# Kernel tuning notes

Hardware: AMD Instinct MI355X
Metric: run time of the kernel (lower is better)

The kernel has to match this reference:

```python
import jax, jax.numpy as jnp
import numpy as np

B, L, D, H = 16, 1024, 768, 12
PHD = D // H  # per-head dim = 64


def setup_inputs() -> dict:
    key = jax.random.key(0)
    ks = jax.random.split(key, 6)
    s = 0.02  # small init scale (xavier-like magnitude)
    return {
        "embeddings": jax.random.normal(ks[0], (B, L, D), jnp.float32),
        "pre_w": jax.random.normal(ks[1], (D, D), jnp.float32) * s,
        "pre_b": jnp.zeros((D,), jnp.float32),
        "psfs": jax.random.normal(ks[2], (H, 2 * L - 1, PHD), jnp.float32) * s,
        "post_w": jax.random.normal(ks[3], (D, D), jnp.float32) * s,
        "post_b": jnp.zeros((D,), jnp.float32),
        "sparse_mat": jax.random.normal(ks[4], (L, L), jnp.float32) * s,
        "ln_g": jnp.ones((D,), jnp.float32),
        "ln_b": jnp.zeros((D,), jnp.float32),
    }


def _spectral_norm(W, n_iters=1, eps=1e-12):
    # torch spectral_norm: power iteration with detached u, v; sigma = u^T W v
    u = jnp.ones((W.shape[0],), W.dtype) / jnp.sqrt(jnp.asarray(W.shape[0], W.dtype))
    for _ in range(n_iters):
        v = W.T @ u
        v = v / (jnp.linalg.norm(v) + eps)
        u = W @ v
        u = u / (jnp.linalg.norm(u) + eps)
    u = jax.lax.stop_gradient(u)
    v = jax.lax.stop_gradient(v)
    sigma = u @ (W @ v)
    return W / sigma


def reference(embeddings, pre_w, pre_b, psfs, post_w, post_b, sparse_mat, ln_g, ln_b):
    # pre-projection
    x = embeddings @ pre_w.T + pre_b                       # (B, L, D)
    # zero-pad along seq to 2L-1 and split heads
    xp = jnp.pad(x, ((0, 0), (0, L - 1), (0, 0)))          # (B, 2L-1, D)
    xp = xp.reshape(B, 2 * L - 1, H, PHD).transpose(0, 2, 1, 3)  # (B, H, 2L-1, d)
    # causal PSF mask: keep first L taps, zero the rest (zeros still enter softmax, as in torch)
    causal = (jnp.arange(2 * L - 1) < L)[None, :, None]
    psf = jnp.where(causal, psfs, 0.0)                     # (H, 2L-1, d)
    psf = jax.nn.softmax(psf, axis=1)
    # 2D circular convolution via FFT over (seq, head_dim)
    conv = jnp.fft.ifftn(jnp.fft.fftn(psf, axes=(1, 2))[None] * jnp.fft.fftn(xp, axes=(2, 3)), axes=(2, 3))
    conv = jnp.real(conv)[:, :, :L, :]                     # (B, H, L, d)
    conv = jax.nn.gelu(conv, approximate=False).transpose(0, 2, 1, 3).reshape(B, L, D)
    conv_emb = conv @ post_w.T + post_b
    # sparse branch: spectrally-normalized, causal-masked dense mixing matrix
    sp = jnp.tril(_spectral_norm(sparse_mat))              # (L, L)
    sparse_emb = jnp.einsum('st,btd->bsd', sp, x)
    # dropout is identity (eval), keep_prob = 1.0; residual + LayerNorm(eps=1e-12)
    y = conv_emb + sparse_emb + embeddings
    mu = jnp.mean(y, axis=-1, keepdims=True)
    var = jnp.mean((y - mu) ** 2, axis=-1, keepdims=True)
    return (y - mu) * jax.lax.rsqrt(var + 1e-12) * ln_g + ln_b
```

## Files before the change

### kernel.cpp

```cpp
#include <hip/hip_runtime.h>
#include <math.h>

#define Bn 16
#define Ln 1024
#define Dn 768
#define Hn 12
#define PHDn 64
#define NK 33
#define NHK (Hn * NK)
#define TWOPI_64 0.09817477042468103f

typedef short s16x8 __attribute__((ext_vector_type(8)));
typedef float f32x4 __attribute__((ext_vector_type(4)));
typedef unsigned short u16x4 __attribute__((ext_vector_type(4)));

__device__ __forceinline__ unsigned short f2bf(float f) {
    unsigned int u = __float_as_uint(f);
    unsigned int r = (u + 0x7FFFu + ((u >> 16) & 1u)) >> 16;
    return (unsigned short)r;
}
__device__ __forceinline__ float bf2f(unsigned short s) {
    unsigned int u = ((unsigned int)s) << 16;
    return __uint_as_float(u);
}
__device__ __forceinline__ float2 cmul(float2 a, float2 b) {
    return make_float2(a.x * b.x - a.y * b.y, a.x * b.y + a.y * b.x);
}

#define SW(j) ((j) ^ (((j) >> 2) & 12) ^ (((j) >> 6) & 3))

static const size_t O_P    = 0;
static const size_t O_PSFH = 786432;
static const size_t O_PART = 1376256;
static const size_t O_QH   = 1597440;
static const size_t O_X    = 1598240;
static const size_t O_XH   = 14181152;
static const size_t O_YH   = 27157280;
static const size_t O_SPE  = 40146080;
static const size_t O_V    = 52728992;
static const size_t O_UR   = 52730016;
static const size_t O_SIG  = 52731040;

__global__ __launch_bounds__(256) void k_psf_softmax(const float* __restrict__ psfs,
                                                     float* __restrict__ p,
                                                     float* __restrict__ q) {
    int he = blockIdx.x;
    int h = he >> 6, e = he & 63;
    int tid = threadIdx.x;
    float ev[4];
    float s = 0.f;
#pragma unroll
    for (int i = 0; i < 4; ++i) {
        int t = tid + 256 * i;
        float v = psfs[((size_t)h * 2047 + t) * 64 + e];
        ev[i] = expf(v);
        s += ev[i];
    }
    __shared__ float red[256];
    red[tid] = s; __syncthreads();
    for (int st = 128; st > 0; st >>= 1) {
        if (tid < st) red[tid] += red[tid + st];
        __syncthreads();
    }
    float denom = red[0] + 1023.0f;
    float inv = 1.0f / denom;
#pragma unroll
    for (int i = 0; i < 4; ++i) {
        int t = tid + 256 * i;
        p[((size_t)h * 1024 + t) * 64 + e] = ev[i] * inv;
    }
    if (tid == 0) q[he] = inv;
}

__global__ __launch_bounds__(256) void k_psf_dft(const float* __restrict__ p,
                                                 float* __restrict__ psfh) {
    int blk = blockIdx.x;
    int h = blk >> 8, tb = blk & 255;
    int t0 = tb * 4;
    int tid = threadIdx.x;
    int w = tid >> 6, lane = tid & 63;
    __shared__ float pv[4][64], cc[64], ssn[64];
    if (tid < 64) {
        float ang = TWOPI_64 * tid;
        cc[tid] = cosf(ang); ssn[tid] = sinf(ang);
    }
    pv[w][lane] = p[((size_t)h * 1024 + t0 + w) * 64 + lane];
    __syncthreads();
    if (lane < NK) {
        float re = 0.f, im = 0.f;
#pragma unroll 8
        for (int e = 0; e < 64; ++e) {
            int j = (lane * e) & 63;
            float v = pv[w][e];
            re += v * cc[j];
            im -= v * ssn[j];
        }
        size_t o = (((size_t)h * NK + lane) * 1024 + t0 + w) * 2;
        psfh[o] = re; psfh[o + 1] = im;
    }
}

__global__ __launch_bounds__(64) void k_q_dft(const float* __restrict__ q,
                                              float* __restrict__ qh) {
    int h = blockIdx.x;
    int tid = threadIdx.x;
    __shared__ float qv[64], cc[64], ssn[64];
    qv[tid] = q[h * 64 + tid];
    float ang = TWOPI_64 * tid;
    cc[tid] = cosf(ang); ssn[tid] = sinf(ang);
    __syncthreads();
    if (tid < NK) {
        float re = 0.f, im = 0.f;
        for (int e = 0; e < 64; ++e) {
            int j = (tid * e) & 63;
            re += qv[e] * cc[j];
            im -= qv[e] * ssn[j];
        }
        qh[(h * NK + tid) * 2] = re;
        qh[(h * NK + tid) * 2 + 1] = im;
    }
}

__device__ __forceinline__ void build_twiddles(float2* tw, int tid) {
#pragma unroll
    for (int it = 0; it < 2; ++it) {
        int j = tid + it * 256;
        float a = (float)j * 3.0679615757712823e-3f;
        float sv, cv;
        __sincosf(a, &sv, &cv);
        tw[j] = make_float2(cv, -sv);
    }
}

__device__ __forceinline__ void fft_pair(const float2* __restrict__ X,
                                         float2* __restrict__ Y,
                                         const float2* __restrict__ tw,
                                         int tid, int m) {
#pragma unroll
    for (int it = 0; it < 2; ++it) {
        int i = tid + it * 256;
        int r = i & (m - 1);
        int am = i - r;
        float2 w1 = tw[am];
        float2 w1b = make_float2(w1.y, -w1.x);
        float2 w2 = cmul(w1, w1);
        float2 x0 = X[SW(i)], x1 = X[SW(i + 512)], x2 = X[SW(i + 1024)], x3 = X[SW(i + 1536)];
        float2 y0 = make_float2(x0.x + x2.x, x0.y + x2.y);
        float2 y1 = cmul(make_float2(x0.x - x2.x, x0.y - x2.y), w1);
        float2 y2 = make_float2(x1.x + x3.x, x1.y + x3.y);
        float2 y3 = cmul(make_float2(x1.x - x3.x, x1.y - x3.y), w1b);
        int o = 4 * am + r;
        Y[SW(o)] = make_float2(y0.x + y2.x, y0.y + y2.y);
        Y[SW(o + m)] = make_float2(y1.x + y3.x, y1.y + y3.y);
        Y[SW(o + 2 * m)] = cmul(make_float2(y0.x - y2.x, y0.y - y2.y), w2);
        Y[SW(o + 3 * m)] = cmul(make_float2(y1.x - y3.x, y1.y - y3.y), w2);
    }
}

__global__ __launch_bounds__(256) void k_tap_fft(const float* __restrict__ psfh,
                                                 const float* __restrict__ qh,
                                                 float* __restrict__ phf) {
    __shared__ float2 A[2048], B[2048], tw[512];
    int hk = blockIdx.x, tid = threadIdx.x;
    build_twiddles(tw, tid);
    float2 qv = make_float2(qh[hk * 2], qh[hk * 2 + 1]);
    const float2* Pg = (const float2*)(psfh + (size_t)hk * 2048);
    __syncthreads();
#pragma unroll
    for (int it = 0; it < 2; ++it) {
        int i = tid + it * 256;
        float2 x0 = Pg[i], x1 = Pg[i + 512];
        float2 x2 = (i == 0) ? make_float2(0.f, 0.f) : qv;
        float2 x3 = qv;
        float2 w1 = tw[i];
        float2 w1b = make_float2(w1.y, -w1.x);
        float2 w2 = cmul(w1, w1);
        float2 y0 = make_float2(x0.x + x2.x, x0.y + x2.y);
        float2 y1 = cmul(make_float2(x0.x - x2.x, x0.y - x2.y), w1);
        float2 y2 = make_float2(x1.x + x3.x, x1.y + x3.y);
        float2 y3 = cmul(make_float2(x1.x - x3.x, x1.y - x3.y), w1b);
        int o = 4 * i;
        A[SW(o)] = make_float2(y0.x + y2.x, y0.y + y2.y);
        A[SW(o + 1)] = make_float2(y1.x + y3.x, y1.y + y3.y);
        A[SW(o + 2)] = cmul(make_float2(y0.x - y2.x, y0.y - y2.y), w2);
        A[SW(o + 3)] = cmul(make_float2(y1.x - y3.x, y1.y - y3.y), w2);
    }
    __syncthreads();
    fft_pair(A, B, tw, tid, 4);   __syncthreads();
    fft_pair(B, A, tw, tid, 16);  __syncthreads();
    fft_pair(A, B, tw, tid, 64);  __syncthreads();
    fft_pair(B, A, tw, tid, 256); __syncthreads();
    float2* out = (float2*)(phf + (size_t)hk * 4096);
#pragma unroll
    for (int it = 0; it < 4; ++it) {
        int t = tid + it * 256;
        float2 lo = A[SW(t)], hi = A[SW(t + 1024)];
        out[t] = make_float2(lo.x + hi.x, lo.y + hi.y);
        out[t + 1024] = make_float2(lo.x - hi.x, lo.y - hi.y);
    }
}

__global__ __launch_bounds__(256) void k_conv_fft(const float* __restrict__ XH,
                                                  const float* __restrict__ PHF,
                                                  float* __restrict__ YH) {
    __shared__ float2 A[2048], B[2048], tw[512];
    int bhk = blockIdx.x, tid = threadIdx.x;
    int hk = bhk % NHK;
    build_twiddles(tw, tid);
    const float2* Xg = (const float2*)(XH + (size_t)bhk * 2048);
    __syncthreads();
#pragma unroll
    for (int it = 0; it < 2; ++it) {
        int i = tid + it * 256;
        float2 x0 = Xg[i];
        float2 x1 = Xg[i + 512];
        float2 w1 = tw[i];
        float2 w1b = make_float2(w1.y, -w1.x);
        float2 w2 = cmul(w1, w1);
        float2 y1 = cmul(x0, w1);
        float2 y3 = cmul(x1, w1b);
        int o = 4 * i;
        A[SW(o)] = make_float2(x0.x + x1.x, x0.y + x1.y);
        A[SW(o + 1)] = make_float2(y1.x + y3.x, y1.y + y3.y);
        A[SW(o + 2)] = cmul(make_float2(x0.x - x1.x, x0.y - x1.y), w2);
        A[SW(o + 3)] = cmul(make_float2(y1.x - y3.x, y1.y - y3.y), w2);
    }
    __syncthreads();
    fft_pair(A, B, tw, tid, 4);   __syncthreads();
    fft_pair(B, A, tw, tid, 16);  __syncthreads();
    fft_pair(A, B, tw, tid, 64);  __syncthreads();
    fft_pair(B, A, tw, tid, 256); __syncthreads();
    const float2* P = (const float2*)(PHF + (size_t)hk * 4096);
    float2 q[8];
#pragma unroll
    for (int it = 0; it < 4; ++it) {
        int t = tid + it * 256;
        float2 lo = A[SW(t)], hi = A[SW(t + 1024)];
        float2 fl = make_float2(lo.x + hi.x, lo.y + hi.y);
        float2 fh = make_float2(lo.x - hi.x, lo.y - hi.y);
        float2 vl = cmul(fl, P[t]);
        float2 vh = cmul(fh, P[t + 1024]);
        q[it] = make_float2(vl.x, -vl.y);
        q[it + 4] = make_float2(vh.x, -vh.y);
    }
#pragma unroll
    for (int it = 0; it < 2; ++it) {
        int i = tid + it * 256;
        float2 x0 = q[it], x1 = q[it + 2], x2 = q[it + 4], x3 = q[it + 6];
        float2 w1 = tw[i];
        float2 w1b = make_float2(w1.y, -w1.x);
        float2 w2 = cmul(w1, w1);
        float2 y0 = make_float2(x0.x + x2.x, x0.y + x2.y);
        float2 y1 = cmul(make_float2(x0.x - x2.x, x0.y - x2.y), w1);
        float2 y2 = make_float2(x1.x + x3.x, x1.y + x3.y);
        float2 y3 = cmul(make_float2(x1.x - x3.x, x1.y - x3.y), w1b);
        int o = 4 * i;
        B[SW(o)] = make_float2(y0.x + y2.x, y0.y + y2.y);
        B[SW(o + 1)] = make_float2(y1.x + y3.x, y1.y + y3.y);
        B[SW(o + 2)] = cmul(make_float2(y0.x - y2.x, y0.y - y2.y), w2);
        B[SW(o + 3)] = cmul(make_float2(y1.x - y3.x, y1.y - y3.y), w2);
    }
    __syncthreads();
    fft_pair(B, A, tw, tid, 4);   __syncthreads();
    fft_pair(A, B, tw, tid, 16);  __syncthreads();
    fft_pair(B, A, tw, tid, 64);  __syncthreads();
    fft_pair(A, B, tw, tid, 256); __syncthreads();
    float2* Yg = (float2*)(YH + (size_t)bhk * 2048);
    const float inv_n = 1.0f / 2048.0f;
#pragma unroll
    for (int it = 0; it < 4; ++it) {
        int s = tid + it * 256;
        float2 lo = B[SW(s)], hi = B[SW(s + 1024)];
        Yg[s] = make_float2((lo.x + hi.x) * inv_n, -(lo.y + hi.y) * inv_n);
    }
}

__global__ __launch_bounds__(64) void k_build_wf1(unsigned short* __restrict__ W) {
    int m = blockIdx.x;
    int d = threadIdx.x;
    float val = 0.f;
    if (m < 66) {
        int k = m >> 1, od = m & 1;
        int j = (k * d) & 63;
        float ang = TWOPI_64 * (float)j;
        val = od ? -sinf(ang) : cosf(ang);
    }
    W[m * 64 + d] = f2bf(val);
}

__global__ __launch_bounds__(64) void k_build_wi1(unsigned short* __restrict__ W) {
    int m = blockIdx.x;
    int c = threadIdx.x;
    float val = 0.f;
    if (m < 64) {
        int d = m;
        int k, od;
        float ck;
        if (c == 0)      { k = 0;  od = 0; ck = 1.f / 64.f; }
        else if (c == 1) { k = 32; od = 0; ck = 1.f / 64.f; }
        else             { k = c >> 1; od = c & 1; ck = 2.f / 64.f; }
        int j = (k * d) & 63;
        float ang = TWOPI_64 * (float)j;
        val = od ? -sinf(ang) * ck : cosf(ang) * ck;
    }
    W[m * 64 + c] = f2bf(val);
}

__device__ __forceinline__ void mfma_core64(const unsigned short* __restrict__ gA0,
                                            const unsigned short* __restrict__ gB0,
                                            int nkt,
                                            unsigned short* __restrict__ As,
                                            unsigned short* __restrict__ Bs,
                                            int tid, int lane, int wr, int wc,
                                            f32x4 acc[4][4]) {
    int r0 = tid >> 1, hs = (tid & 1) << 2;
    int wbase = r0 * 64;
    int swr = r0 & 7;
    int kg = lane >> 4, cl = lane & 15;
    int fra[8], frb[8];
#pragma unroll
    for (int kk = 0; kk < 2; ++kk)
#pragma unroll
        for (int i = 0; i < 4; ++i) {
            int ra = wr * 64 + i * 16 + cl;
            fra[kk * 4 + i] = ra * 64 + (((kk * 4 + kg) ^ (ra & 7)) << 3);
            int rb = wc * 64 + i * 16 + cl;
            frb[kk * 4 + i] = rb * 64 + (((kk * 4 + kg) ^ (rb & 7)) << 3);
        }
    s16x8 a[4], b[4];
#pragma unroll
    for (int l = 0; l < 4; ++l) {
        a[l] = *(const s16x8*)(gA0 + l * 8);
        b[l] = *(const s16x8*)(gB0 + l * 8);
    }
    for (int kt = 0; kt < nkt; ++kt) {
        __syncthreads();
#pragma unroll
        for (int l = 0; l < 4; ++l) {
            *(s16x8*)&As[wbase + (((hs + l) ^ swr) << 3)] = a[l];
            *(s16x8*)&Bs[wbase + (((hs + l) ^ swr) << 3)] = b[l];
        }
        __syncthreads();
        if (kt + 1 < nkt) {
            size_t ko = (size_t)(kt + 1) * 64;
#pragma unroll
            for (int l = 0; l < 4; ++l) {
                a[l] = *(const s16x8*)(gA0 + ko + l * 8);
                b[l] = *(const s16x8*)(gB0 + ko + l * 8);
            }
        }
#pragma unroll
        for (int kk = 0; kk < 2; ++kk) {
            s16x8 af[4], bfr[4];
#pragma unroll
            for (int i = 0; i < 4; ++i) af[i] = *(const s16x8*)&As[fra[kk * 4 + i]];
#pragma unroll
            for (int i = 0; i < 4; ++i) bfr[i] = *(const s16x8*)&Bs[frb[kk * 4 + i]];
#pragma unroll
            for (int mi = 0; mi < 4; ++mi)
#pragma unroll
                for (int ni = 0; ni < 4; ++ni)
                    acc[mi][ni] = __builtin_amdgcn_mfma_f32_16x16x32_bf16(af[mi], bfr[ni], acc[mi][ni], 0, 0, 0);
        }
    }
}

__global__ __launch_bounds__(256) void k_mfma_abt_bf(const unsigned short* __restrict__ A,
                                                     const unsigned short* __restrict__ W,
                                                     const float* __restrict__ bias,
                                                     unsigned short* __restrict__ C,
                                                     int M, int N, int K) {
    int n0 = blockIdx.x * 128, m0 = blockIdx.y * 128;
    int tid = threadIdx.x;
    int lane = tid & 63, wave = tid >> 6;
    int wr = wave >> 1, wc = wave & 1;
    __shared__ __align__(16) unsigned short As[8192], Bs[8192];
    f32x4 acc[4][4] = {};
    int r0 = tid >> 1, hs = (tid & 1) << 2;
    const unsigned short* gA0 = A + (size_t)(m0 + r0) * K + hs * 8;
    const unsigned short* gB0 = W + (size_t)(n0 + r0) * K + hs * 8;
    mfma_core64(gA0, gB0, K >> 6, As, Bs, tid, lane, wr, wc, acc);
    int kg = lane >> 4, cl = lane & 15;
#pragma unroll
    for (int ni = 0; ni < 4; ++ni) {
        int gn = n0 + wc * 64 + ni * 16 + cl;
        float bv = bias ? bias[gn] : 0.f;
#pragma unroll
        for (int mi = 0; mi < 4; ++mi) {
            int gm = m0 + wr * 64 + mi * 16 + kg * 4;
            f32x4 v = acc[mi][ni];
#pragma unroll
            for (int ri = 0; ri < 4; ++ri)
                C[(size_t)(gm + ri) * N + gn] = f2bf(v[ri] + bv);
        }
    }
}

__global__ __launch_bounds__(256) void k_mfma_dft_h(const unsigned short* __restrict__ Wf1,
                                                    const unsigned short* __restrict__ Xb,
                                                    float* __restrict__ XH) {
    int n0 = blockIdx.x * 128;
    int h = blockIdx.y;
    int tid = threadIdx.x;
    int lane = tid & 63, wave = tid >> 6;
    int wr = wave >> 1, wc = wave & 1;
    __shared__ __align__(16) unsigned short As[8192], Bs[8192];
    f32x4 acc[4][4] = {};
    int r0 = tid >> 1, hs = (tid & 1) << 2;
    const unsigned short* gA0 = Wf1 + r0 * 64 + hs * 8;
    const unsigned short* gB0 = Xb + (size_t)(n0 + r0) * Dn + h * 64 + hs * 8;
    mfma_core64(gA0, gB0, 1, As, Bs, tid, lane, wr, wc, acc);
    int kg = lane >> 4, cl = lane & 15;
#pragma unroll
    for (int ni = 0; ni < 4; ++ni) {
        int gn = n0 + wc * 64 + ni * 16 + cl;
        int b = gn >> 10, u = gn & 1023;
#pragma unroll
        for (int mi = 0; mi < 4; ++mi) {
            int gmb = wr * 64 + mi * 16 + kg * 4;
            f32x4 v = acc[mi][ni];
#pragma unroll
            for (int rp = 0; rp < 2; ++rp) {
                int m = gmb + rp * 2;
                if (m < 66) {
                    size_t plane = (size_t)(b * Hn + h) * NK + (m >> 1);
                    *(float2*)&XH[(plane * 1024 + u) * 2] = make_float2(v[rp * 2], v[rp * 2 + 1]);
                }
            }
        }
    }
}

__global__ __launch_bounds__(256) void k_transpose_yh(const float* __restrict__ YH,
                                                      unsigned short* __restrict__ YT) {
    int ut = blockIdx.x & 7;
    int h = (blockIdx.x >> 3) % 12;
    int b = blockIdx.x / 96;
    int u0 = ut * 128;
    __shared__ unsigned short T[128 * 66];
    int tid = threadIdx.x;
    int planeBase = (b * Hn + h) * NK;
    const float2* Yg = (const float2*)YH;
#pragma unroll
    for (int i = 0; i < 17; ++i) {
        int idx = tid + i * 256;
        if (idx < 4224) {
            int k = idx >> 7, uo = idx & 127;
            float2 v = Yg[(size_t)(planeBase + k) * 1024 + u0 + uo];
            T[uo * 66 + 2 * k] = f2bf(v.x);
            T[uo * 66 + 2 * k + 1] = f2bf(v.y);
        }
    }
    __syncthreads();
    unsigned int* out = (unsigned int*)YT;
#pragma unroll
    for (int i = 0; i < 16; ++i) {
        int idx = tid + i * 256;
        int uo = idx >> 5, w = idx & 31;
        unsigned int lo, hi;
        if (w == 0) {
            lo = T[uo * 66 + 0];
            hi = T[uo * 66 + 64];
        } else {
            lo = T[uo * 66 + 2 * w];
            hi = T[uo * 66 + 2 * w + 1];
        }
        size_t r = (size_t)b * 1024 + u0 + uo;
        out[r * 384 + h * 32 + w] = lo | (hi << 16);
    }
}

__global__ __launch_bounds__(256) void k_mfma_idft_h(const unsigned short* __restrict__ YT,
                                                     const unsigned short* __restrict__ Wi1,
                                                     unsigned short* __restrict__ G) {
    int m0 = blockIdx.x * 128;
    int h = blockIdx.y;
    int tid = threadIdx.x;
    int lane = tid & 63, wave = tid >> 6;
    int wr = wave >> 1, wc = wave & 1;
    __shared__ __align__(16) unsigned short As[8192], Bs[8192];
    f32x4 acc[4][4] = {};
    int r0 = tid >> 1, hs = (tid & 1) << 2;
    const unsigned short* gA0 = YT + (size_t)(m0 + r0) * Dn + h * 64 + hs * 8;
    const unsigned short* gB0 = Wi1 + r0 * 64 + hs * 8;
    mfma_core64(gA0, gB0, 1, As, Bs, tid, lane, wr, wc, acc);
    int kg = lane >> 4, cl = lane & 15;
#pragma unroll
    for (int ni = 0; ni < 4; ++ni) {
        int gn = wc * 64 + ni * 16 + cl;
        if (gn < 64) {
#pragma unroll
            for (int mi = 0; mi < 4; ++mi) {
                int gm = m0 + wr * 64 + mi * 16 + kg * 4;
                f32x4 v = acc[mi][ni];
#pragma unroll
                for (int ri = 0; ri < 4; ++ri) {
                    float c = v[ri];
                    float g = c * 0.5f * (1.0f + erff(c * 0.70710678118f));
                    G[(size_t)(gm + ri) * Dn + h * 64 + gn] = f2bf(g);
                }
            }
        }
    }
}

__global__ __launch_bounds__(256) void k_mfma_sparse(const unsigned short* __restrict__ SP,
                                                     const unsigned short* __restrict__ XT,
                                                     const float* __restrict__ sigbuf,
                                                     unsigned short* __restrict__ C) {
    int bx = blockIdx.x;
    int mt = bx & 7, nt = (bx >> 3) % 6, b = bx / 48;
    int m0 = mt * 128, n0 = nt * 128;
    const unsigned short* Xb = XT + (size_t)b * Dn * Ln;
    unsigned short* Cb = C + (size_t)b * Ln * Dn;
    int tid = threadIdx.x;
    int lane = tid & 63, wave = tid >> 6;
    int wr = wave >> 1, wc = wave & 1;
    __shared__ __align__(16) unsigned short As[8192], Bs[8192];
    f32x4 acc[4][4] = {};
    int r0 = tid >> 1, hs = (tid & 1) << 2;
    const unsigned short* gA0 = SP + (size_t)(m0 + r0) * Ln + hs * 8;
    const unsigned short* gB0 = Xb + (size_t)(n0 + r0) * Ln + hs * 8;
    mfma_core64(gA0, gB0, 2 * mt + 2, As, Bs, tid, lane, wr, wc, acc);
    float invs = sigbuf[0];
    int kg = lane >> 4, cl = lane & 15;
#pragma unroll
    for (int ni = 0; ni < 4; ++ni) {
        int gn = n0 + wc * 64 + ni * 16 + cl;
#pragma unroll
        for (int mi = 0; mi < 4; ++mi) {
            int gm = m0 + wr * 64 + mi * 16 + kg * 4;
            f32x4 v = acc[mi][ni];
#pragma unroll
            for (int ri = 0; ri < 4; ++ri)
                Cb[(size_t)(gm + ri) * Dn + gn] = f2bf(v[ri] * invs);
        }
    }
}

__global__ __launch_bounds__(256) void k_cvt_bf16(const float* __restrict__ in,
                                                  unsigned short* __restrict__ out, int n4) {
    int i = blockIdx.x * 256 + threadIdx.x;
    if (i < n4) {
        float4 v = ((const float4*)in)[i];
        u16x4 o;
        o[0] = f2bf(v.x); o[1] = f2bf(v.y); o[2] = f2bf(v.z); o[3] = f2bf(v.w);
        *(u16x4*)&out[(size_t)i * 4] = o;
    }
}

__global__ __launch_bounds__(256) void k_cvt_sp(const float* __restrict__ SP,
                                                unsigned short* __restrict__ O) {
    int s = blockIdx.x;
    int t0 = threadIdx.x * 4;
    float4 v = *(const float4*)&SP[(size_t)s * 1024 + t0];
    u16x4 o;
    o[0] = (t0 + 0 <= s) ? f2bf(v.x) : 0;
    o[1] = (t0 + 1 <= s) ? f2bf(v.y) : 0;
    o[2] = (t0 + 2 <= s) ? f2bf(v.z) : 0;
    o[3] = (t0 + 3 <= s) ? f2bf(v.w) : 0;
    *(u16x4*)&O[(size_t)s * 1024 + t0] = o;
}

__global__ __launch_bounds__(256) void k_transpose_x(const unsigned short* __restrict__ X,
                                                     unsigned short* __restrict__ XT) {
    int d0 = blockIdx.x * 64, t0 = blockIdx.y * 64, b = blockIdx.z;
    const unsigned short* Xb = X + (size_t)b * Ln * Dn;
    unsigned short* Tb = XT + (size_t)b * Dn * Ln;
    __shared__ unsigned short tile[64 * 65];
    int tx = threadIdx.x & 63, ty = threadIdx.x >> 6;
#pragma unroll
    for (int i = 0; i < 16; ++i) {
        int t = ty + i * 4;
        tile[t * 65 + tx] = Xb[(size_t)(t0 + t) * Dn + d0 + tx];
    }
    __syncthreads();
#pragma unroll
    for (int i = 0; i < 16; ++i) {
        int d = ty + i * 4;
        Tb[(size_t)(d0 + d) * Ln + t0 + tx] = tile[tx * 65 + d];
    }
}

__global__ __launch_bounds__(256) void k_sn_colsum(const float* __restrict__ Wm,
                                                   float* __restrict__ partial) {
    int b = blockIdx.x;
    int tid = threadIdx.x;
    int c0 = tid * 4;
    float4 s = make_float4(0.f, 0.f, 0.f, 0.f);
#pragma unroll
    for (int i = 0; i < 16; ++i) {
        float4 v = *(const float4*)&Wm[(size_t)(b * 16 + i) * 1024 + c0];
        s.x += v.x; s.y += v.y; s.z += v.z; s.w += v.w;
    }
    *(float4*)&partial[(size_t)b * 1024 + c0] = s;
}

__global__ __launch_bounds__(1024) void k_sn_v2(const float* __restrict__ partial,
                                                float* __restrict__ v) {
    int j = threadIdx.x;
    float s = 0.f;
#pragma unroll 8
    for (int i = 0; i < 64; ++i) s += partial[(size_t)i * 1024 + j];
    s *= 0.03125f;
    __shared__ float red[1024];
    red[j] = s * s; __syncthreads();
    for (int st = 512; st > 0; st >>= 1) {
        if (j < st) red[j] += red[j + st];
        __syncthreads();
    }
    float nrm = sqrtf(red[0]);
    v[j] = s / (nrm + 1e-12f);
}

__global__ __launch_bounds__(64) void k_sn_u(const float* __restrict__ Wm,
                                             const float* __restrict__ v,
                                             float* __restrict__ ur) {
    int i = blockIdx.x;
    int lane = threadIdx.x;
    float s = 0.f;
    for (int j = lane; j < 1024; j += 64) s += Wm[(size_t)i * 1024 + j] * v[j];
#pragma unroll
    for (int off = 32; off > 0; off >>= 1) s += __shfl_down(s, off);
    if (lane == 0) ur[i] = s;
}

__global__ __launch_bounds__(1024) void k_sn_sigma(const float* __restrict__ ur,
                                                   float* __restrict__ sig) {
    int i = threadIdx.x;
    __shared__ float red[1024];
    float u = ur[i];
    red[i] = u * u; __syncthreads();
    for (int st = 512; st > 0; st >>= 1) {
        if (i < st) red[i] += red[i + st];
        __syncthreads();
    }
    if (i == 0) {
        float ss = red[0];
        float sigma = ss / (sqrtf(ss) + 1e-12f);
        sig[0] = 1.0f / sigma;
    }
}

__global__ __launch_bounds__(256) void k_final_ln(const unsigned short* __restrict__ CE,
                                                  const unsigned short* __restrict__ SE,
                                                  const float* __restrict__ EMB,
                                                  const float* __restrict__ g,
                                                  const float* __restrict__ be,
                                                  float* __restrict__ out) {
    int r = blockIdx.x;
    int tid = threadIdx.x;
    float y[3];
    float s = 0.f;
#pragma unroll
    for (int i = 0; i < 3; ++i) {
        int o = tid + i * 256;
        size_t idx = (size_t)r * 768 + o;
        y[i] = bf2f(CE[idx]) + bf2f(SE[idx]) + EMB[idx];
        s += y[i];
    }
    __shared__ float red[256];
    red[tid] = s; __syncthreads();
    for (int st = 128; st > 0; st >>= 1) {
        if (tid < st) red[tid] += red[tid + st];
        __syncthreads();
    }
    float mu = red[0] * (1.f / 768.f);
    __syncthreads();
    float vs = 0.f;
#pragma unroll
    for (int i = 0; i < 3; ++i) { float d = y[i] - mu; vs += d * d; }
    red[tid] = vs; __syncthreads();
    for (int st = 128; st > 0; st >>= 1) {
        if (tid < st) red[tid] += red[tid + st];
        __syncthreads();
    }
    float var = red[0] * (1.f / 768.f);
    float rstd = rsqrtf(var + 1e-12f);
#pragma unroll
    for (int i = 0; i < 3; ++i) {
        int o = tid + i * 256;
        size_t idx = (size_t)r * 768 + o;
        out[idx] = (y[i] - mu) * rstd * g[o] + be[o];
    }
}

extern "C" void kernel_launch(void* const* d_in, const int* in_sizes, int n_in,
                              void* d_out, int out_size, void* d_ws, size_t ws_size,
                              hipStream_t stream) {
    const float* emb     = (const float*)d_in[0];
    const float* pre_w   = (const float*)d_in[1];
    const float* pre_b   = (const float*)d_in[2];
    const float* psfs    = (const float*)d_in[3];
    const float* post_w  = (const float*)d_in[4];
    const float* post_b  = (const float*)d_in[5];
    const float* spmat   = (const float*)d_in[6];
    const float* ln_g    = (const float*)d_in[7];
    const float* ln_b    = (const float*)d_in[8];
    float* out = (float*)d_out;
    float* ws = (float*)d_ws;

    float* p      = ws + O_P;
    float* psfh   = ws + O_PSFH;
    float* part   = ws + O_PART;
    float* qh     = ws + O_QH;
    float* q      = ws + O_SIG + 8;
    float* XH     = ws + O_XH;
    float* YH     = ws + O_YH;
    float* phf    = ws + O_SPE;
    float* v      = ws + O_V;
    float* urw    = ws + O_UR;
    float* sig    = ws + O_SIG;

    unsigned short* x_bf      = (unsigned short*)(ws + O_X);
    unsigned short* Wf1       = (unsigned short*)(ws + O_X + 6291456);
    unsigned short* Wi1       = (unsigned short*)(ws + O_X + 6295552);
    unsigned short* YT        = (unsigned short*)(ws + O_XH);
    unsigned short* xT_bf     = (unsigned short*)(ws + O_XH);
    unsigned short* emb_bf    = (unsigned short*)(ws + O_YH);
    unsigned short* CE_bf     = (unsigned short*)(ws + O_YH);
    unsigned short* spe_bf    = (unsigned short*)(ws + O_SPE);
    unsigned short* G_bf      = (unsigned short*)(ws + O_SPE + 3145728);
    unsigned short* SP_bf     = (unsigned short*)(ws + O_P);
    unsigned short* pre_w_bf  = (unsigned short*)(ws + O_PSFH);
    unsigned short* post_w_bf = (unsigned short*)(ws + O_PSFH + 294912);

    k_psf_softmax<<<Hn * 64, 256, 0, stream>>>(psfs, p, q);
    k_psf_dft<<<Hn * 256, 256, 0, stream>>>(p, psfh);
    k_q_dft<<<Hn, 64, 0, stream>>>(q, qh);
    k_tap_fft<<<NHK, 256, 0, stream>>>(psfh, qh, phf);

    k_sn_colsum<<<64, 256, 0, stream>>>(spmat, part);
    k_sn_v2<<<1, 1024, 0, stream>>>(part, v);
    k_sn_u<<<1024, 64, 0, stream>>>(spmat, v, urw);
    k_sn_sigma<<<1, 1024, 0, stream>>>(urw, sig);

    k_cvt_sp<<<1024, 256, 0, stream>>>(spmat, SP_bf);
    k_cvt_bf16<<<576, 256, 0, stream>>>(pre_w, pre_w_bf, 147456);
    k_cvt_bf16<<<576, 256, 0, stream>>>(post_w, post_w_bf, 147456);
    k_cvt_bf16<<<12288, 256, 0, stream>>>(emb, emb_bf, 3145728);
    k_build_wf1<<<128, 64, 0, stream>>>(Wf1);
    k_build_wi1<<<128, 64, 0, stream>>>(Wi1);

    k_mfma_abt_bf<<<dim3(6, 128), 256, 0, stream>>>(emb_bf, pre_w_bf, pre_b, x_bf, Bn * Ln, Dn, Dn);

    k_mfma_dft_h<<<dim3(128, Hn), 256, 0, stream>>>(Wf1, x_bf, XH);

    k_conv_fft<<<Bn * NHK, 256, 0, stream>>>(XH, phf, YH);

    k_transpose_yh<<<Bn * Hn * 8, 256, 0, stream>>>(YH, YT);

    k_mfma_idft_h<<<dim3(128, Hn), 256, 0, stream>>>(YT, Wi1, G_bf);

    k_transpose_x<<<dim3(12, 16, Bn), 256, 0, stream>>>(x_bf, xT_bf);

    k_mfma_abt_bf<<<dim3(6, 128), 256, 0, stream>>>(G_bf, post_w_bf, post_b, CE_bf, Bn * Ln, Dn, Dn);

    k_mfma_sparse<<<768, 256, 0, stream>>>(SP_bf, xT_bf, sig, spe_bf);

    k_final_ln<<<Bn * Ln, 256, 0, stream>>>(CE_bf, spe_bf, emb, ln_g, ln_b, out);
}
```

Baseline: 319.5 us.

## Store FFT spectra as packed bf16 and fuse fp32→bf16 conversion into GEMM loads

Intermediate frequency-domain buffers XH and YH are now stored as packed bf16 complex pairs instead of float2, halving the memory traffic of the DFT, convolution FFT and transpose kernels. The separate fp32-to-bf16 conversion kernels for embeddings and the pre/post weights are removed; the GEMM loaders read fp32 directly and convert in registers. This trades extra spectral rounding error and some redundant fp32 global reads for fewer kernel launches and less intermediate traffic.

```diff
diff --git a/kernel.cpp b/kernel.cpp
--- a/kernel.cpp
+++ b/kernel.cpp
@@ -25,6 +25,12 @@
 }
 __device__ __forceinline__ float2 cmul(float2 a, float2 b) {
     return make_float2(a.x * b.x - a.y * b.y, a.x * b.y + a.y * b.x);
+}
+__device__ __forceinline__ unsigned int packbf(float re, float im) {
+    return (unsigned int)f2bf(re) | ((unsigned int)f2bf(im) << 16);
+}
+__device__ __forceinline__ float2 unpackbf(unsigned int v) {
+    return make_float2(bf2f((unsigned short)(v & 0xffff)), bf2f((unsigned short)(v >> 16)));
 }
 
 #define SW(j) ((j) ^ (((j) >> 2) & 12) ^ (((j) >> 6) & 3))
@@ -200,20 +206,20 @@
     }
 }
 
-__global__ __launch_bounds__(256) void k_conv_fft(const float* __restrict__ XH,
+__global__ __launch_bounds__(256) void k_conv_fft(const unsigned int* __restrict__ XHb,
                                                   const float* __restrict__ PHF,
-                                                  float* __restrict__ YH) {
+                                                  unsigned int* __restrict__ YHb) {
     __shared__ float2 A[2048], B[2048], tw[512];
     int bhk = blockIdx.x, tid = threadIdx.x;
     int hk = bhk % NHK;
     build_twiddles(tw, tid);
-    const float2* Xg = (const float2*)(XH + (size_t)bhk * 2048);
+    const unsigned int* Xg = XHb + (size_t)bhk * 1024;
     __syncthreads();
 #pragma unroll
     for (int it = 0; it < 2; ++it) {
         int i = tid + it * 256;
-        float2 x0 = Xg[i];
-        float2 x1 = Xg[i + 512];
+        float2 x0 = unpackbf(Xg[i]);
+        float2 x1 = unpackbf(Xg[i + 512]);
         float2 w1 = tw[i];
         float2 w1b = make_float2(w1.y, -w1.x);
         float2 w2 = cmul(w1, w1);
@@ -265,13 +271,13 @@
     fft_pair(A, B, tw, tid, 16);  __syncthreads();
     fft_pair(B, A, tw, tid, 64);  __syncthreads();
     fft_pair(A, B, tw, tid, 256); __syncthreads();
-    float2* Yg = (float2*)(YH + (size_t)bhk * 2048);
+    unsigned int* Yg = YHb + (size_t)bhk * 1024;
     const float inv_n = 1.0f / 2048.0f;
 #pragma unroll
     for (int it = 0; it < 4; ++it) {
         int s = tid + it * 256;
         float2 lo = B[SW(s)], hi = B[SW(s + 1024)];
-        Yg[s] = make_float2((lo.x + hi.x) * inv_n, -(lo.y + hi.y) * inv_n);
+        Yg[s] = packbf((lo.x + hi.x) * inv_n, -(lo.y + hi.y) * inv_n);
     }
 }
 
@@ -306,8 +312,19 @@
     W[m * 64 + c] = f2bf(val);
 }
 
-__device__ __forceinline__ void mfma_core64(const unsigned short* __restrict__ gA0,
-                                            const unsigned short* __restrict__ gB0,
+__device__ __forceinline__ s16x8 load8(const unsigned short* p) { return *(const s16x8*)p; }
+__device__ __forceinline__ s16x8 load8(const float* p) {
+    float4 u = *(const float4*)p;
+    float4 v = *(const float4*)(p + 4);
+    s16x8 r;
+    r[0] = (short)f2bf(u.x); r[1] = (short)f2bf(u.y); r[2] = (short)f2bf(u.z); r[3] = (short)f2bf(u.w);
+    r[4] = (short)f2bf(v.x); r[5] = (short)f2bf(v.y); r[6] = (short)f2bf(v.z); r[7] = (short)f2bf(v.w);
+    return r;
+}
+
+template <typename TA, typename TB>
+__device__ __forceinline__ void mfma_core64(const TA* __restrict__ gA0,
+                                            const TB* __restrict__ gB0,
                                             int nkt,
                                             unsigned short* __restrict__ As,
                                             unsigned short* __restrict__ Bs,
@@ -330,8 +347,8 @@
     s16x8 a[4], b[4];
 #pragma unroll
     for (int l = 0; l < 4; ++l) {
-        a[l] = *(const s16x8*)(gA0 + l * 8);
-        b[l] = *(const s16x8*)(gB0 + l * 8);
+        a[l] = load8(gA0 + l * 8);
+        b[l] = load8(gB0 + l * 8);
     }
     for (int kt = 0; kt < nkt; ++kt) {
         __syncthreads();
@@ -345,8 +362,8 @@
             size_t ko = (size_t)(kt + 1) * 64;
 #pragma unroll
             for (int l = 0; l < 4; ++l) {
-                a[l] = *(const s16x8*)(gA0 + ko + l * 8);
-                b[l] = *(const s16x8*)(gB0 + ko + l * 8);
+                a[l] = load8(gA0 + ko + l * 8);
+                b[l] = load8(gB0 + ko + l * 8);
             }
         }
 #pragma unroll
@@ -365,11 +382,42 @@
     }
 }
 
-__global__ __launch_bounds__(256) void k_mfma_abt_bf(const unsigned short* __restrict__ A,
-                                                     const unsigned short* __restrict__ W,
-                                                     const float* __restrict__ bias,
-                                                     unsigned short* __restrict__ C,
-                                                     int M, int N, int K) {
+__global__ __launch_bounds__(256) void k_mfma_pre(const float* __restrict__ A,
+                                                  const float* __restrict__ W,
+                                                  const float* __restrict__ bias,
+                                                  unsigned short* __restrict__ C) {
+    const int K = Dn, N = Dn;
+    int n0 = blockIdx.x * 128, m0 = blockIdx.y * 128;
+    int tid = threadIdx.x;
+    int lane = tid & 63, wave = tid >> 6;
+    int wr = wave >> 1, wc = wave & 1;
+    __shared__ __align__(16) unsigned short As[8192], Bs[8192];
+    f32x4 acc[4][4] = {};
+    int r0 = tid >> 1, hs = (tid & 1) << 2;
+    const float* gA0 = A + (size_t)(m0 + r0) * K + hs * 8;
+    const float* gB0 = W + (size_t)(n0 + r0) * K + hs * 8;
+    mfma_core64(gA0, gB0, K >> 6, As, Bs, tid, lane, wr, wc, acc);
+    int kg = lane >> 4, cl = lane & 15;
+#pragma unroll
+    for (int ni = 0; ni < 4; ++ni) {
+        int gn = n0 + wc * 64 + ni * 16 + cl;
+        float bv = bias[gn];
+#pragma unroll
+        for (int mi = 0; mi < 4; ++mi) {
+            int gm = m0 + wr * 64 + mi * 16 + kg * 4;
+            f32x4 v = acc[mi][ni];
+#pragma unroll
+            for (int ri = 0; ri < 4; ++ri)
+                C[(size_t)(gm + ri) * N + gn] = f2bf(v[ri] + bv);
+        }
+    }
+}
+
+__global__ __launch_bounds__(256) void k_mfma_post(const unsigned short* __restrict__ A,
+                                                   const float* __restrict__ W,
+                                                   const float* __restrict__ bias,
+                                                   unsigned short* __restrict__ C) {
+    const int K = Dn, N = Dn;
     int n0 = blockIdx.x * 128, m0 = blockIdx.y * 128;
     int tid = threadIdx.x;
     int lane = tid & 63, wave = tid >> 6;
@@ -378,13 +426,13 @@
     f32x4 acc[4][4] = {};
     int r0 = tid >> 1, hs = (tid & 1) << 2;
     const unsigned short* gA0 = A + (size_t)(m0 + r0) * K + hs * 8;
-    const unsigned short* gB0 = W + (size_t)(n0 + r0) * K + hs * 8;
+    const float* gB0 = W + (size_t)(n0 + r0) * K + hs * 8;
     mfma_core64(gA0, gB0, K >> 6, As, Bs, tid, lane, wr, wc, acc);
     int kg = lane >> 4, cl = lane & 15;
 #pragma unroll
     for (int ni = 0; ni < 4; ++ni) {
         int gn = n0 + wc * 64 + ni * 16 + cl;
-        float bv = bias ? bias[gn] : 0.f;
+        float bv = bias[gn];
 #pragma unroll
         for (int mi = 0; mi < 4; ++mi) {
             int gm = m0 + wr * 64 + mi * 16 + kg * 4;
@@ -398,7 +446,7 @@
 
 __global__ __launch_bounds__(256) void k_mfma_dft_h(const unsigned short* __restrict__ Wf1,
                                                     const unsigned short* __restrict__ Xb,
-                                                    float* __restrict__ XH) {
+                                                    unsigned int* __restrict__ XHb) {
     int n0 = blockIdx.x * 128;
     int h = blockIdx.y;
     int tid = threadIdx.x;
@@ -424,14 +472,14 @@
                 int m = gmb + rp * 2;
                 if (m < 66) {
                     size_t plane = (size_t)(b * Hn + h) * NK + (m >> 1);
-                    *(float2*)&XH[(plane * 1024 + u) * 2] = make_float2(v[rp * 2], v[rp * 2 + 1]);
+                    XHb[plane * 1024 + u] = packbf(v[rp * 2], v[rp * 2 + 1]);
                 }
             }
         }
     }
 }
 
-__global__ __launch_bounds__(256) void k_transpose_yh(const float* __restrict__ YH,
+__global__ __launch_bounds__(256) void k_transpose_yh(const unsigned int* __restrict__ YHb,
                                                       unsigned short* __restrict__ YT) {
     int ut = blockIdx.x & 7;
     int h = (blockIdx.x >> 3) % 12;
@@ -440,15 +488,14 @@
     __shared__ unsigned short T[128 * 66];
     int tid = threadIdx.x;
     int planeBase = (b * Hn + h) * NK;
-    const float2* Yg = (const float2*)YH;
 #pragma unroll
     for (int i = 0; i < 17; ++i) {
         int idx = tid + i * 256;
         if (idx < 4224) {
             int k = idx >> 7, uo = idx & 127;
-            float2 v = Yg[(size_t)(planeBase + k) * 1024 + u0 + uo];
-            T[uo * 66 + 2 * k] = f2bf(v.x);
-            T[uo * 66 + 2 * k + 1] = f2bf(v.y);
+            unsigned int v = YHb[(size_t)(planeBase + k) * 1024 + u0 + uo];
+            T[uo * 66 + 2 * k] = (unsigned short)(v & 0xffff);
+            T[uo * 66 + 2 * k + 1] = (unsigned short)(v >> 16);
         }
     }
     __syncthreads();
@@ -535,17 +582,6 @@
             for (int ri = 0; ri < 4; ++ri)
                 Cb[(size_t)(gm + ri) * Dn + gn] = f2bf(v[ri] * invs);
         }
-    }
-}
-
-__global__ __launch_bounds__(256) void k_cvt_bf16(const float* __restrict__ in,
-                                                  unsigned short* __restrict__ out, int n4) {
-    int i = blockIdx.x * 256 + threadIdx.x;
-    if (i < n4) {
-        float4 v = ((const float4*)in)[i];
-        u16x4 o;
-        o[0] = f2bf(v.x); o[1] = f2bf(v.y); o[2] = f2bf(v.z); o[3] = f2bf(v.w);
-        *(u16x4*)&out[(size_t)i * 4] = o;
     }
 }
 
@@ -705,8 +741,8 @@
     float* part   = ws + O_PART;
     float* qh     = ws + O_QH;
     float* q      = ws + O_SIG + 8;
-    float* XH     = ws + O_XH;
-    float* YH     = ws + O_YH;
+    unsigned int* XHb = (unsigned int*)(ws + O_XH);
+    unsigned int* YHb = (unsigned int*)(ws + O_YH);
     float* phf    = ws + O_SPE;
     float* v      = ws + O_V;
     float* urw    = ws + O_UR;
@@ -717,13 +753,10 @@
     unsigned short* Wi1       = (unsigned short*)(ws + O_X + 6295552);
     unsigned short* YT        = (unsigned short*)(ws + O_XH);
     unsigned short* xT_bf     = (unsigned short*)(ws + O_XH);
-    unsigned short* emb_bf    = (unsigned short*)(ws + O_YH);
     unsigned short* CE_bf     = (unsigned short*)(ws + O_YH);
     unsigned short* spe_bf    = (unsigned short*)(ws + O_SPE);
     unsigned short* G_bf      = (unsigned short*)(ws + O_SPE + 3145728);
     unsigned short* SP_bf     = (unsigned short*)(ws + O_P);
-    unsigned short* pre_w_bf  = (unsigned short*)(ws + O_PSFH);
-    unsigned short* post_w_bf = (unsigned short*)(ws + O_PSFH + 294912);
 
     k_psf_softmax<<<Hn * 64, 256, 0, stream>>>(psfs, p, q);
     k_psf_dft<<<Hn * 256, 256, 0, stream>>>(p, psfh);
@@ -736,25 +769,22 @@
     k_sn_sigma<<<1, 1024, 0, stream>>>(urw, sig);
 
     k_cvt_sp<<<1024, 256, 0, stream>>>(spmat, SP_bf);
-    k_cvt_bf16<<<576, 256, 0, stream>>>(pre_w, pre_w_bf, 147456);
-    k_cvt_bf16<<<576, 256, 0, stream>>>(post_w, post_w_bf, 147456);
-    k_cvt_bf16<<<12288, 256, 0, stream>>>(emb, emb_bf, 3145728);
     k_build_wf1<<<128, 64, 0, stream>>>(Wf1);
     k_build_wi1<<<128, 64, 0, stream>>>(Wi1);
 
-    k_mfma_abt_bf<<<dim3(6, 128), 256, 0, stream>>>(emb_bf, pre_w_bf, pre_b, x_bf, Bn * Ln, Dn, Dn);
-
-    k_mfma_dft_h<<<dim3(128, Hn), 256, 0, stream>>>(Wf1, x_bf, XH);
-
-    k_conv_fft<<<Bn * NHK, 256, 0, stream>>>(XH, phf, YH);
-
-    k_transpose_yh<<<Bn * Hn * 8, 256, 0, stream>>>(YH, YT);
+    k_mfma_pre<<<dim3(6, 128), 256, 0, stream>>>(emb, pre_w, pre_b, x_bf);
+
+    k_mfma_dft_h<<<dim3(128, Hn), 256, 0, stream>>>(Wf1, x_bf, XHb);
+
+    k_conv_fft<<<Bn * NHK, 256, 0, stream>>>(XHb, phf, YHb);
+
+    k_transpose_yh<<<Bn * Hn * 8, 256, 0, stream>>>(YHb, YT);
 
     k_mfma_idft_h<<<dim3(128, Hn), 256, 0, stream>>>(YT, Wi1, G_bf);
 
     k_transpose_x<<<dim3(12, 16, Bn), 256, 0, stream>>>(x_bf, xT_bf);
 
-    k_mfma_abt_bf<<<dim3(6, 128), 256, 0, stream>>>(G_bf, post_w_bf, post_b, CE_bf, Bn * Ln, Dn, Dn);
+    k_mfma_post<<<dim3(6, 128), 256, 0, stream>>>(G_bf, post_w, post_b, CE_bf);
 
     k_mfma_sparse<<<768, 256, 0, stream>>>(SP_bf, xT_bf, sig, spe_bf);
 
```

Result: slower. 377.7 us (+18.2%).
